# Optimization experiments

Measured on AMD Instinct MI355X. Metric: run time of the kernel, lower is better.

## Reference

```python
import jax, jax.numpy as jnp
import numpy as np

N, E, G = 50000, 500000, 2048
HID, H, ED, L = 128, 4, 12, 8
D = HID // H
EPS_BN = 1e-5


def setup_inputs() -> dict:
    key = jax.random.key(0)
    ks = jax.random.split(key, 32)
    s = 0.05
    x = jax.random.normal(ks[0], (N, 22), jnp.float32)
    src = jax.random.randint(ks[1], (E,), 0, N)
    off = jax.random.randint(ks[2], (E,), 1, N)
    dst = (src + off) % N  # guaranteed no self-loops -> move_mask is all True
    batch = jnp.sort(jax.random.randint(ks[3], (N,), 0, G))
    edge_attr = jax.random.normal(ks[4], (E, ED), jnp.float32)
    params = dict(
        Win=jax.random.normal(ks[5], (22, HID), jnp.float32) * s,
        b_in=jnp.zeros((HID,), jnp.float32),
        Wl=jax.random.normal(ks[6], (L, HID, HID), jnp.float32) * s,
        bl=jnp.zeros((L, HID), jnp.float32),
        Wr=jax.random.normal(ks[7], (L, HID, HID), jnp.float32) * s,
        br=jnp.zeros((L, HID), jnp.float32),
        We=jax.random.normal(ks[8], (L, ED, HID), jnp.float32) * s,
        att=jax.random.normal(ks[9], (L, H, D), jnp.float32) * s,
        bo=jnp.zeros((L, HID), jnp.float32),
        gamma=jnp.ones((L, HID), jnp.float32),
        beta=jnp.zeros((L, HID), jnp.float32),
        Wv1=jax.random.normal(ks[10], (HID, 64), jnp.float32) * s,
        bv1=jnp.zeros((64,), jnp.float32),
        Wv2=jax.random.normal(ks[11], (64, 3), jnp.float32) * s,
        bv2=jnp.zeros((3,), jnp.float32),
        Wp1=jax.random.normal(ks[12], (2 * HID + ED, 64), jnp.float32) * s,
        bp1=jnp.zeros((64,), jnp.float32),
        Wp2=jax.random.normal(ks[13], (64, 1), jnp.float32) * s,
        bp2=jnp.zeros((1,), jnp.float32),
    )
    return dict(x=x, src=src, dst=dst, batch=batch, edge_attr=edge_attr, **params)


def _bn(h, g, b):
    mu = h.mean(0)
    var = h.var(0)
    return (h - mu) * jax.lax.rsqrt(var + EPS_BN) * g + b


def _gatv2(h, src, dst, edge_attr, Wl, bl, Wr, br, We, att, bo):
    xl = (h @ Wl + bl).reshape(N, H, D)   # source-side (values + score)
    xr = (h @ Wr + br).reshape(N, H, D)   # target-side (score)
    e = (edge_attr @ We).reshape(E, H, D)
    sc = xl[src] + xr[dst] + e            # [E,H,D]
    sc = jnp.where(sc > 0, sc, 0.2 * sc)  # LeakyReLU(0.2)
    a = jnp.einsum('ehd,hd->eh', sc, att)  # [E,H]
    m = jax.ops.segment_max(a, dst, num_segments=N)
    ex = jnp.exp(a - m[dst])
    den = jax.ops.segment_sum(ex, dst, num_segments=N)
    alpha = ex / (den[dst] + 1e-16)        # per-destination softmax
    out = jax.ops.segment_sum(xl[src] * alpha[..., None], dst, num_segments=N)
    return out.reshape(N, HID) + bo


def reference(x, src, dst, batch, edge_attr, Win, b_in, Wl, bl, Wr, br, We, att,
              bo, gamma, beta, Wv1, bv1, Wv2, bv2, Wp1, bp1, Wp2, bp2):
    h = jax.nn.relu(x @ Win + b_in)
    for blk in range(L // 2):
        i, j = 2 * blk, 2 * blk + 1
        res = h
        h = jax.nn.relu(_bn(_gatv2(h, src, dst, edge_attr, Wl[i], bl[i], Wr[i], br[i], We[i], att[i], bo[i]), gamma[i], beta[i]))
        h = _bn(_gatv2(h, src, dst, edge_attr, Wl[j], bl[j], Wr[j], br[j], We[j], att[j], bo[j]), gamma[j], beta[j])
        h = jax.nn.relu(h + res)
    cnt = jax.ops.segment_sum(jnp.ones((N,), h.dtype), batch, num_segments=G)
    pooled = jax.ops.segment_sum(h, batch, num_segments=G) / jnp.maximum(cnt, 1.0)[:, None]
    value_logits = jax.nn.relu(pooled @ Wv1 + bv1) @ Wv2 + bv2   # [G,3]
    edge_in = jnp.concatenate([h[src], h[dst], edge_attr], axis=1)  # [E, 2*HID+ED]
    policy_logits = (jax.nn.relu(edge_in @ Wp1 + bp1) @ Wp2 + bp2)[:, 0]  # [E]
    return (value_logits, policy_logits)
```

## Files before the change

kernel.cpp:

```cpp
#include <hip/hip_runtime.h>
#include <math.h>

#define N_NODES 50000
#define N_EDGES 500000
#define N_GRAPHS 2048
#define HID 128
#define EDIM 12
#define NLAYERS 8
#define EPS_BN 1e-5f
#define LOG2E 1.44269504088896340736f

typedef __attribute__((ext_vector_type(8))) short short8;
typedef __attribute__((ext_vector_type(4))) float f32x4;
typedef __attribute__((ext_vector_type(2))) float f32x2;
typedef unsigned int uint;
typedef unsigned short ushort;

__device__ inline ushort f2bf(float x) {
  unsigned u = __float_as_uint(x);
  u = (u + 0x7FFFu + ((u >> 16) & 1u)) >> 16;
  return (ushort)u;
}
__device__ inline unsigned pk_bf16(float a, float b) {
  return (unsigned)f2bf(a) | ((unsigned)f2bf(b) << 16);
}
__device__ inline float bflo(uint q) { return __uint_as_float(q << 16); }
__device__ inline float bfhi(uint q) { return __uint_as_float(q & 0xFFFF0000u); }
__device__ inline f32x2 pfma(f32x2 a, f32x2 b, f32x2 c) {
  return __builtin_elementwise_fma(a, b, c);
}
template <int CTRL>
__device__ inline float dpp_add(float v) {
  int s = __builtin_amdgcn_update_dpp(0, __float_as_int(v), CTRL, 0xF, 0xF, true);
  return v + __int_as_float(s);
}
#define RED8(v)               \
  v = dpp_add<0xB1>(v);       \
  v = dpp_add<0x4E>(v);       \
  v = dpp_add<0x141>(v);

__global__ void zero_kernel(int* deg, int* cursor, float* stats, uint* erec) {
  int i = blockIdx.x * 256 + threadIdx.x;
  if (i < N_NODES) { deg[i] = 0; cursor[i] = 0; }
  if (i < NLAYERS * 256) stats[i] = 0.f;
  if (i < 32) erec[(size_t)N_EDGES * 8 + i] = 0u;
}

__global__ void count_kernel(const int* __restrict__ dst, int* __restrict__ deg) {
  int e = blockIdx.x * 256 + threadIdx.x;
  if (e < N_EDGES) atomicAdd(&deg[dst[e]], 1);
}

__global__ void scan1_kernel(int* __restrict__ off, int* __restrict__ bsum) {
  __shared__ int s[256];
  int t = threadIdx.x; int n = blockIdx.x * 256 + t;
  int x = (n < N_NODES) ? off[n] : 0;
  s[t] = x; __syncthreads();
  for (int o = 1; o < 256; o <<= 1) {
    int v = (t >= o) ? s[t - o] : 0;
    __syncthreads(); s[t] += v; __syncthreads();
  }
  if (n < N_NODES) off[n] = s[t] - x;
  if (t == 255) bsum[blockIdx.x] = s[255];
}

__global__ void scan2_kernel(int* __restrict__ bsum, int nb) {
  __shared__ int s[256];
  int t = threadIdx.x;
  int x = (t < nb) ? bsum[t] : 0;
  s[t] = x; __syncthreads();
  for (int o = 1; o < 256; o <<= 1) {
    int v = (t >= o) ? s[t - o] : 0;
    __syncthreads(); s[t] += v; __syncthreads();
  }
  if (t < nb) bsum[t] = s[t] - x;
}

__global__ void scan3_kernel(int* __restrict__ off, const int* __restrict__ bsum) {
  int t = threadIdx.x; int n = blockIdx.x * 256 + t;
  if (n < N_NODES) off[n] += bsum[blockIdx.x];
  if (n == 0 && blockIdx.x == 0) off[N_NODES] = N_EDGES;
}

__global__ void scatter_kernel(const int* __restrict__ src, const int* __restrict__ dst,
                               const float* __restrict__ ea,
                               const int* __restrict__ off, int* __restrict__ cursor,
                               uint* __restrict__ erec) {
  int e = blockIdx.x * 256 + threadIdx.x;
  if (e < N_EDGES) {
    int d = dst[e];
    int p = atomicAdd(&cursor[d], 1);
    int pos = off[d] + p;
    const float* eap = &ea[(size_t)e * EDIM];
    float4 e0 = *(const float4*)eap;
    float4 e1 = *(const float4*)(eap + 4);
    float4 e2 = *(const float4*)(eap + 8);
    uint4 q0, q1;
    q0.x = (uint)src[e]; q0.y = 0u;
    q0.z = pk_bf16(e0.x, e0.y); q0.w = pk_bf16(e0.z, e0.w);
    q1.x = pk_bf16(e1.x, e1.y); q1.y = pk_bf16(e1.z, e1.w);
    q1.z = pk_bf16(e2.x, e2.y); q1.w = pk_bf16(e2.z, e2.w);
    uint* o = &erec[(size_t)pos * 8];
    *(uint4*)o = q0;
    *(uint4*)(o + 4) = q1;
  }
}

__global__ void wprep_kernel(const float* __restrict__ Wl, const float* __restrict__ Wr,
                             ushort* __restrict__ wpk) {
  int idx = blockIdx.x * 256 + threadIdx.x;
  if (idx >= NLAYERS * 4 * 256 * 32) return;
  int kk = idx & 31;
  int cc = (idx >> 5) & 255;
  int kb = (idx >> 13) & 3;
  int layer = idx >> 15;
  int k = kb * 32 + kk;
  float v = (cc < 128) ? Wl[((size_t)layer * 128 + k) * 128 + cc]
                       : Wr[((size_t)layer * 128 + k) * 128 + (cc - 128)];
  wpk[idx] = f2bf(v);
}

__global__ void wprep_pol_kernel(const float* __restrict__ Wp1, ushort* __restrict__ wppk) {
  int idx = blockIdx.x * 256 + threadIdx.x;
  if (idx >= 4 * 128 * 32) return;
  int kk = idx & 31;
  int cc = (idx >> 5) & 127;
  int kb = idx >> 12;
  int k = kb * 32 + kk;
  float v = (cc < 64) ? Wp1[(size_t)k * 64 + cc] : Wp1[(size_t)(128 + k) * 64 + (cc - 64)];
  wppk[idx] = f2bf(v);
}

__global__ void inproj_kernel(const float* __restrict__ x, const float* __restrict__ Win,
                              const float* __restrict__ b_in, float* __restrict__ h,
                              ushort* __restrict__ h16) {
  __shared__ float xs[44];
  int t = threadIdx.x;
  int n0 = blockIdx.x * 2;
  if (t < 44) xs[t] = x[n0 * 22 + t];
  __syncthreads();
  int c = t & 127, half = t >> 7;
  int n = n0 + half;
  if (n < N_NODES) {
    float acc = b_in[c];
#pragma unroll
    for (int k = 0; k < 22; k++) acc = fmaf(xs[half * 22 + k], Win[k * HID + c], acc);
    float v = fmaxf(acc, 0.f);
    h[(size_t)n * HID + c] = v;
    h16[(size_t)n * HID + c] = f2bf(v);
  }
}

template <int NOUT, int SPLIT, bool BIAS, bool OUTBF16, bool BNFUSE, bool RESID, bool WRITEH>
__global__ __launch_bounds__(256) void gemm_mfma_kernel(
    const ushort* __restrict__ A16, const ushort* __restrict__ T16,
    const float* __restrict__ stats, const float* __restrict__ gamma,
    const float* __restrict__ beta, const float* __restrict__ res,
    float* __restrict__ hout,
    const ushort* __restrict__ Wpk, const float* __restrict__ b1,
    const float* __restrict__ b2, void* __restrict__ C1v, void* __restrict__ C2v,
    int nrows) {
  __shared__ ushort As[64][136];
  int t = threadIdx.x;
  int brow = blockIdx.x * 64;
  if constexpr (!BNFUSE) {
#pragma unroll
    for (int i = 0; i < 4; i++) {
      int f = t + i * 256;
      int r = f >> 4, cg = (f & 15) * 8;
      int g = brow + r;
      uint4 v = make_uint4(0, 0, 0, 0);
      if (g < nrows) v = *(const uint4*)&A16[(size_t)g * HID + cg];
      *(uint4*)&As[r][cg] = v;
    }
  } else {
    int cg = (t & 31) * 4;
    int r0 = t >> 5;
    const float invN = 1.f / (float)N_NODES;
    float4 sm = *(const float4*)&stats[cg];
    float4 sq = *(const float4*)&stats[128 + cg];
    float4 gm = *(const float4*)&gamma[cg];
    float4 bt = *(const float4*)&beta[cg];
    float s4[4] = {sm.x, sm.y, sm.z, sm.w};
    float q4[4] = {sq.x, sq.y, sq.z, sq.w};
    float g4[4] = {gm.x, gm.y, gm.z, gm.w};
    float bb4[4] = {bt.x, bt.y, bt.z, bt.w};
    float scl[4], shf[4];
#pragma unroll
    for (int k = 0; k < 4; k++) {
      float mu = s4[k] * invN;
      float var = q4[k] * invN - mu * mu;
      float rs = rsqrtf(var + EPS_BN);
      scl[k] = g4[k] * rs;
      shf[k] = bb4[k] - mu * scl[k];
    }
#pragma unroll
    for (int rr = 0; rr < 8; rr++) {
      int r = r0 + rr * 8;
      int g = brow + r;
      uint2 tvu = make_uint2(0u, 0u);
      if (g < nrows) tvu = *(const uint2*)&T16[(size_t)g * HID + cg];
      float o0 = fmaf(bflo(tvu.x), scl[0], shf[0]);
      float o1 = fmaf(bfhi(tvu.x), scl[1], shf[1]);
      float o2 = fmaf(bflo(tvu.y), scl[2], shf[2]);
      float o3 = fmaf(bfhi(tvu.y), scl[3], shf[3]);
      if constexpr (RESID) {
        if (g < nrows) {
          float4 rv = *(const float4*)&res[(size_t)g * HID + cg];
          o0 += rv.x; o1 += rv.y; o2 += rv.z; o3 += rv.w;
        }
      }
      o0 = fmaxf(o0, 0.f); o1 = fmaxf(o1, 0.f);
      o2 = fmaxf(o2, 0.f); o3 = fmaxf(o3, 0.f);
      if constexpr (WRITEH) {
        if (g < nrows) {
          float4 ov = make_float4(o0, o1, o2, o3);
          *(float4*)&hout[(size_t)g * HID + cg] = ov;
        }
      }
      *(uint2*)&As[r][cg] = make_uint2(pk_bf16(o0, o1), pk_bf16(o2, o3));
    }
  }
  __syncthreads();
  int lane = t & 63, wave = t >> 6;
  int arow = wave * 16 + (lane & 15);
  int k8 = (lane >> 4) * 8;
  constexpr int NT = NOUT / 16;
  f32x4 acc[NT];
#pragma unroll
  for (int n = 0; n < NT; n++) acc[n] = (f32x4){0.f, 0.f, 0.f, 0.f};
#pragma unroll
  for (int kb = 0; kb < 4; kb++) {
    short8 a = *(const short8*)&As[arow][kb * 32 + k8];
#pragma unroll
    for (int n = 0; n < NT; n++) {
      int col = n * 16 + (lane & 15);
      short8 b = *(const short8*)&Wpk[((size_t)(kb * NOUT + col)) * 32 + k8];
      acc[n] = __builtin_amdgcn_mfma_f32_16x16x32_bf16(a, b, acc[n], 0, 0, 0);
    }
  }
  int rbase = brow + wave * 16 + (lane >> 4) * 4;
  int ccol = lane & 15;
#pragma unroll
  for (int n = 0; n < NT; n++) {
    int col = n * 16 + ccol;
    float bias = 0.f;
    if (BIAS) bias = (col < SPLIT) ? b1[col] : b2[col - SPLIT];
    int colw = (col < SPLIT) ? col : col - SPLIT;
#pragma unroll
    for (int j = 0; j < 4; j++) {
      int row = rbase + j;
      if (row < nrows) {
        float v = acc[n][j] + bias;
        if (OUTBF16) {
          ushort* dstp = (ushort*)((col < SPLIT) ? C1v : C2v);
          dstp[(size_t)row * SPLIT + colw] = f2bf(v);
        } else {
          float* dstp = (float*)((col < SPLIT) ? C1v : C2v);
          dstp[(size_t)row * SPLIT + colw] = v;
        }
      }
    }
  }
}

#define GAT_EDGE4(ra, rb, xw, OKEXPR)                                        \
  {                                                                          \
    f32x2 xa01 = (f32x2){bflo(xw.x), bfhi(xw.x)};                            \
    f32x2 xa23 = (f32x2){bflo(xw.y), bfhi(xw.y)};                            \
    f32x2 ep01 = xa01 + xr01;                                                \
    f32x2 ep23 = xa23 + xr23;                                                \
    uint q; float lo, hi;                                                    \
    q = ra.z; lo = bflo(q); hi = bfhi(q);                                    \
    ep01 = pfma((f32x2){lo, lo}, wk01[0], ep01);                             \
    ep23 = pfma((f32x2){lo, lo}, wk23[0], ep23);                             \
    ep01 = pfma((f32x2){hi, hi}, wk01[1], ep01);                             \
    ep23 = pfma((f32x2){hi, hi}, wk23[1], ep23);                             \
    q = ra.w; lo = bflo(q); hi = bfhi(q);                                    \
    ep01 = pfma((f32x2){lo, lo}, wk01[2], ep01);                             \
    ep23 = pfma((f32x2){lo, lo}, wk23[2], ep23);                             \
    ep01 = pfma((f32x2){hi, hi}, wk01[3], ep01);                             \
    ep23 = pfma((f32x2){hi, hi}, wk23[3], ep23);                             \
    q = rb.x; lo = bflo(q); hi = bfhi(q);                                    \
    ep01 = pfma((f32x2){lo, lo}, wk01[4], ep01);                             \
    ep23 = pfma((f32x2){lo, lo}, wk23[4], ep23);                             \
    ep01 = pfma((f32x2){hi, hi}, wk01[5], ep01);                             \
    ep23 = pfma((f32x2){hi, hi}, wk23[5], ep23);                             \
    q = rb.y; lo = bflo(q); hi = bfhi(q);                                    \
    ep01 = pfma((f32x2){lo, lo}, wk01[6], ep01);                             \
    ep23 = pfma((f32x2){lo, lo}, wk23[6], ep23);                             \
    ep01 = pfma((f32x2){hi, hi}, wk01[7], ep01);                             \
    ep23 = pfma((f32x2){hi, hi}, wk23[7], ep23);                             \
    q = rb.z; lo = bflo(q); hi = bfhi(q);                                    \
    ep01 = pfma((f32x2){lo, lo}, wk01[8], ep01);                             \
    ep23 = pfma((f32x2){lo, lo}, wk23[8], ep23);                             \
    ep01 = pfma((f32x2){hi, hi}, wk01[9], ep01);                             \
    ep23 = pfma((f32x2){hi, hi}, wk23[9], ep23);                             \
    q = rb.w; lo = bflo(q); hi = bfhi(q);                                    \
    ep01 = pfma((f32x2){lo, lo}, wk01[10], ep01);                            \
    ep23 = pfma((f32x2){lo, lo}, wk23[10], ep23);                            \
    ep01 = pfma((f32x2){hi, hi}, wk01[11], ep01);                            \
    ep23 = pfma((f32x2){hi, hi}, wk23[11], ep23);                            \
    f32x2 s01 = __builtin_elementwise_max(ep01, ep01 * (f32x2){0.2f, 0.2f}); \
    f32x2 s23 = __builtin_elementwise_max(ep23, ep23 * (f32x2){0.2f, 0.2f}); \
    float v = fmaf(s01.x, at4.x,                                             \
              fmaf(s01.y, at4.y, fmaf(s23.x, at4.z, s23.y * at4.w)));        \
    RED8(v)                                                                  \
    bool ok = (OKEXPR);                                                      \
    float dm = v - m;                                                        \
    float e = __builtin_amdgcn_exp2f(-fabsf(dm));                            \
    bool big = dm > 0.f;                                                     \
    float sc = (big && ok) ? e : 1.f;                                        \
    float p = ok ? (big ? 1.f : e) : 0.f;                                    \
    m = (ok && big) ? v : m;                                                 \
    d = fmaf(d, sc, p);                                                      \
    acc01 = pfma(acc01, (f32x2){sc, sc}, (f32x2){p, p} * xa01);              \
    acc23 = pfma(acc23, (f32x2){sc, sc}, (f32x2){p, p} * xa23);              \
  }

__global__ __launch_bounds__(256, 4) void gat_kernel(
    const ushort* __restrict__ xl16, const ushort* __restrict__ xr16,
    const uint* __restrict__ erec, const int* __restrict__ off,
    const float* __restrict__ Wel, const float* __restrict__ attl,
    const float* __restrict__ bol, ushort* __restrict__ out16) {
  int lane = threadIdx.x & 63;
  int node = blockIdx.x * 4 + (threadIdx.x >> 6);
  if (node >= N_NODES) return;
  int half = lane >> 5;
  int c0 = (lane & 31) * 4;

  f32x2 wk01[12], wk23[12];
#pragma unroll
  for (int k = 0; k < 12; k++) {
    float4 w = *(const float4*)&Wel[k * HID + c0];
    wk01[k] = (f32x2){w.x, w.y};
    wk23[k] = (f32x2){w.z, w.w};
  }
  float4 at4 = *(const float4*)&attl[c0];
  at4.x *= LOG2E; at4.y *= LOG2E; at4.z *= LOG2E; at4.w *= LOG2E;
  uint2 xru = *(const uint2*)&xr16[((uint)node << 7) + c0];
  f32x2 xr01 = (f32x2){bflo(xru.x), bfhi(xru.x)};
  f32x2 xr23 = (f32x2){bflo(xru.y), bfhi(xru.y)};

  int is = off[node], deg = off[node + 1] - is;

  float m = -INFINITY, d = 0.f;
  f32x2 acc01 = (f32x2){0.f, 0.f};
  f32x2 acc23 = (f32x2){0.f, 0.f};

  if (deg > 0) {
    const uint* pe = erec + ((size_t)is + half) * 8;
    uint4 Ra = *(const uint4*)pe, Rb = *(const uint4*)(pe + 4);
    uint2 xw = *(const uint2*)&xl16[(Ra.x << 7) + c0];
    int full = deg >> 1;
    for (int i = 0; i < full; i++) {
      const uint* pn = pe + 16;
      uint4 Na = *(const uint4*)pn, Nb = *(const uint4*)(pn + 4);
      uint2 xn = *(const uint2*)&xl16[(Na.x << 7) + c0];
      GAT_EDGE4(Ra, Rb, xw, true)
      Ra = Na; Rb = Nb; xw = xn; pe = pn;
    }
    if (deg & 1) GAT_EDGE4(Ra, Rb, xw, half == 0)
  }

  float mo = __shfl_xor(m, 32);
  float dd = __shfl_xor(d, 32);
  f32x2 o01, o23;
  o01.x = __shfl_xor(acc01.x, 32); o01.y = __shfl_xor(acc01.y, 32);
  o23.x = __shfl_xor(acc23.x, 32); o23.y = __shfl_xor(acc23.y, 32);
  float mn = fmaxf(m, mo);
  float wS = (m > -INFINITY) ? __builtin_amdgcn_exp2f(m - mn) : 0.f;
  float wO = (mo > -INFINITY) ? __builtin_amdgcn_exp2f(mo - mn) : 0.f;
  float den = d * wS + dd * wO;
  f32x2 a01 = acc01 * (f32x2){wS, wS} + o01 * (f32x2){wO, wO};
  f32x2 a23 = acc23 * (f32x2){wS, wS} + o23 * (f32x2){wO, wO};
  float inv = 1.f / (den + 1e-16f);
  if (half == 0) {
    float4 bo = *(const float4*)&bol[c0];
    uint2 o;
    o.x = pk_bf16(fmaf(a01.x, inv, bo.x), fmaf(a01.y, inv, bo.y));
    o.y = pk_bf16(fmaf(a23.x, inv, bo.z), fmaf(a23.y, inv, bo.w));
    *(uint2*)&out16[((uint)node << 7) + c0] = o;
  }
}

__global__ void bnstats_kernel(const ushort* __restrict__ t16, float* __restrict__ sums) {
  int tid = threadIdx.x;
  int c2 = (tid & 63) * 2;
  int grp = tid >> 6;
  float s0 = 0.f, s1 = 0.f, q0 = 0.f, q1 = 0.f;
  for (int n = blockIdx.x * 4 + grp; n < N_NODES; n += 1024) {
    uint v = *(const uint*)&t16[((uint)n << 7) + c2];
    float a = bflo(v), b = bfhi(v);
    s0 += a; q0 = fmaf(a, a, q0);
    s1 += b; q1 = fmaf(b, b, q1);
  }
  __shared__ float ls[4][128], lq[4][128];
  *(float2*)&ls[grp][c2] = make_float2(s0, s1);
  *(float2*)&lq[grp][c2] = make_float2(q0, q1);
  __syncthreads();
  if (tid < 128) {
    float s = ls[0][tid] + ls[1][tid] + ls[2][tid] + ls[3][tid];
    atomicAdd(&sums[tid], s);
    float q = lq[0][tid] + lq[1][tid] + lq[2][tid] + lq[3][tid];
    atomicAdd(&sums[128 + tid], q);
  }
}

__global__ __launch_bounds__(256) void policy_kernel(
    const ushort* __restrict__ Ps, const ushort* __restrict__ Pd,
    const int* __restrict__ src, const int* __restrict__ dst,
    const float* __restrict__ edge_attr, const float* __restrict__ Wp1e,
    const float* __restrict__ bp1, const float* __restrict__ Wp2,
    const float* __restrict__ bp2, float* __restrict__ outp) {
  int j = threadIdx.x & 15;
  int gid = (blockIdx.x * 256 + threadIdx.x) >> 4;
  int ngroups = (gridDim.x * 256) >> 4;
  float4 we[12];
#pragma unroll
  for (int k = 0; k < 12; k++) we[k] = *(const float4*)&Wp1e[k * 64 + j * 4];
  float4 b4 = *(const float4*)&bp1[j * 4];
  float4 w2 = *(const float4*)&Wp2[j * 4];
  float bp2c = bp2[0];
  for (int e = gid; e < N_EDGES; e += ngroups) {
    int s = src[e], d = dst[e];
    const float* eap = &edge_attr[(size_t)e * EDIM];
    float4 e0 = *(const float4*)eap;
    float4 e1 = *(const float4*)(eap + 4);
    float4 e2 = *(const float4*)(eap + 8);
    uint2 psu = *(const uint2*)&Ps[(size_t)s * 64 + j * 4];
    uint2 pdu = *(const uint2*)&Pd[(size_t)d * 64 + j * 4];
    float eav[12] = {e0.x, e0.y, e0.z, e0.w, e1.x, e1.y, e1.z, e1.w, e2.x, e2.y, e2.z, e2.w};
    float hx = bflo(psu.x) + bflo(pdu.x) + b4.x;
    float hy = bfhi(psu.x) + bfhi(pdu.x) + b4.y;
    float hz = bflo(psu.y) + bflo(pdu.y) + b4.z;
    float hw = bfhi(psu.y) + bfhi(pdu.y) + b4.w;
#pragma unroll
    for (int k = 0; k < 12; k++) {
      hx = fmaf(eav[k], we[k].x, hx);
      hy = fmaf(eav[k], we[k].y, hy);
      hz = fmaf(eav[k], we[k].z, hz);
      hw = fmaf(eav[k], we[k].w, hw);
    }
    hx = fmaxf(hx, 0.f); hy = fmaxf(hy, 0.f); hz = fmaxf(hz, 0.f); hw = fmaxf(hw, 0.f);
    float v = fmaf(hx, w2.x, fmaf(hy, w2.y, fmaf(hz, w2.z, hw * w2.w)));
    v += __shfl_xor(v, 1);
    v += __shfl_xor(v, 2);
    v += __shfl_xor(v, 4);
    v += __shfl_xor(v, 8);
    if (j == 0) outp[e] = v + bp2c;
  }
}

__device__ int lower_bound_dev(const int* a, int n, int key) {
  int lo = 0, hi = n;
  while (lo < hi) {
    int mid = (lo + hi) >> 1;
    if (a[mid] < key) lo = mid + 1; else hi = mid;
  }
  return lo;
}

__global__ void poolvalue_kernel(const float* __restrict__ h, const int* __restrict__ batch,
                                 const float* __restrict__ Wv1, const float* __restrict__ bv1,
                                 const float* __restrict__ Wv2, const float* __restrict__ bv2,
                                 float* __restrict__ outv) {
  __shared__ float pl[128];
  __shared__ float hd[64];
  __shared__ int range[2];
  int g = blockIdx.x, t = threadIdx.x;
  if (t == 0) {
    range[0] = lower_bound_dev(batch, N_NODES, g);
    range[1] = lower_bound_dev(batch, N_NODES, g + 1);
  }
  __syncthreads();
  int lo = range[0], hi = range[1];
  float s = 0.f;
  for (int n = lo; n < hi; n++) s += h[(size_t)n * HID + t];
  float cnt = (float)(hi - lo);
  pl[t] = s / fmaxf(cnt, 1.f);
  __syncthreads();
  if (t < 64) {
    float a = bv1[t];
    for (int c = 0; c < 128; c++) a = fmaf(pl[c], Wv1[c * 64 + t], a);
    hd[t] = fmaxf(a, 0.f);
  }
  __syncthreads();
  if (t < 3) {
    float a = bv2[t];
    for (int j = 0; j < 64; j++) a = fmaf(hd[j], Wv2[j * 3 + t], a);
    outv[g * 3 + t] = a;
  }
}

extern "C" void kernel_launch(void* const* d_in, const int* in_sizes, int n_in,
                              void* d_out, int out_size, void* d_ws, size_t ws_size,
                              hipStream_t stream) {
  (void)in_sizes; (void)n_in; (void)out_size; (void)ws_size;
  const float* x    = (const float*)d_in[0];
  const int*   src  = (const int*)d_in[1];
  const int*   dst  = (const int*)d_in[2];
  const int*   batch= (const int*)d_in[3];
  const float* ea   = (const float*)d_in[4];
  const float* Win  = (const float*)d_in[5];
  const float* b_in = (const float*)d_in[6];
  const float* Wl   = (const float*)d_in[7];
  const float* bl   = (const float*)d_in[8];
  const float* Wr   = (const float*)d_in[9];
  const float* br   = (const float*)d_in[10];
  const float* We   = (const float*)d_in[11];
  const float* att  = (const float*)d_in[12];
  const float* bo   = (const float*)d_in[13];
  const float* gamma= (const float*)d_in[14];
  const float* beta = (const float*)d_in[15];
  const float* Wv1  = (const float*)d_in[16];
  const float* bv1  = (const float*)d_in[17];
  const float* Wv2  = (const float*)d_in[18];
  const float* bv2  = (const float*)d_in[19];
  const float* Wp1  = (const float*)d_in[20];
  const float* bp1  = (const float*)d_in[21];
  const float* Wp2  = (const float*)d_in[22];
  const float* bp2  = (const float*)d_in[23];

  float* outv = (float*)d_out;
  float* outp = outv + (size_t)N_GRAPHS * 3;

  float* hres   = (float*)d_ws;
  ushort* tmp16 = (ushort*)(hres + (size_t)N_NODES * HID);
  ushort* h16   = tmp16 + (size_t)N_NODES * HID;
  ushort* xl16  = h16 + (size_t)N_NODES * HID;
  ushort* xr16  = xl16 + (size_t)N_NODES * HID;
  float* stats  = (float*)(xr16 + (size_t)N_NODES * HID);
  ushort* wpk   = (ushort*)(stats + NLAYERS * 256);
  ushort* wppk  = wpk + (size_t)NLAYERS * 4 * 256 * 32;
  int* off    = (int*)(wppk + 4 * 128 * 32);
  int* cursor = off + (N_NODES + 1);
  int* bsum   = cursor + N_NODES;
  uint* erec  = (uint*)(((uintptr_t)(bsum + 256) + 15) & ~(uintptr_t)15);

  const int NB = (N_NODES + 255) / 256;
  const int EB = (N_EDGES + 255) / 256;

  zero_kernel<<<NB, 256, 0, stream>>>(off, cursor, stats, erec);
  count_kernel<<<EB, 256, 0, stream>>>(dst, off);
  scan1_kernel<<<NB, 256, 0, stream>>>(off, bsum);
  scan2_kernel<<<1, 256, 0, stream>>>(bsum, NB);
  scan3_kernel<<<NB, 256, 0, stream>>>(off, bsum);
  scatter_kernel<<<EB, 256, 0, stream>>>(src, dst, ea, off, cursor, erec);
  wprep_kernel<<<(NLAYERS * 4 * 256 * 32 + 255) / 256, 256, 0, stream>>>(Wl, Wr, wpk);
  wprep_pol_kernel<<<(4 * 128 * 32 + 255) / 256, 256, 0, stream>>>(Wp1, wppk);
  inproj_kernel<<<N_NODES / 2, 256, 0, stream>>>(x, Win, b_in, hres, h16);

  const int MB = (N_NODES + 63) / 64;
  const int GATB = (N_NODES + 3) / 4;

  for (int l = 0; l < NLAYERS; l++) {
    if (l == 0) {
      gemm_mfma_kernel<256, 128, true, true, false, false, false><<<MB, 256, 0, stream>>>(
          h16, nullptr, nullptr, nullptr, nullptr, nullptr, nullptr,
          wpk, bl, br, xl16, xr16, N_NODES);
    } else if (l & 1) {
      int p = l - 1;
      gemm_mfma_kernel<256, 128, true, true, true, false, false><<<MB, 256, 0, stream>>>(
          nullptr, tmp16, stats + p * 256, gamma + p * HID, beta + p * HID, nullptr, nullptr,
          wpk + (size_t)l * 32768, bl + l * HID, br + l * HID, xl16, xr16, N_NODES);
    } else {
      int p = l - 1;
      gemm_mfma_kernel<256, 128, true, true, true, true, true><<<MB, 256, 0, stream>>>(
          nullptr, tmp16, stats + p * 256, gamma + p * HID, beta + p * HID, hres, hres,
          wpk + (size_t)l * 32768, bl + l * HID, br + l * HID, xl16, xr16, N_NODES);
    }
    gat_kernel<<<GATB, 256, 0, stream>>>(xl16, xr16, erec, off,
                                         We + (size_t)l * EDIM * HID, att + (size_t)l * HID,
                                         bo + (size_t)l * HID, tmp16);
    bnstats_kernel<<<256, 256, 0, stream>>>(tmp16, stats + l * 256);
  }

  ushort* Ps = xl16;
  ushort* Pd = xr16;
  gemm_mfma_kernel<128, 64, false, true, true, true, true><<<MB, 256, 0, stream>>>(
      nullptr, tmp16, stats + 7 * 256, gamma + 7 * HID, beta + 7 * HID, hres, hres,
      wppk, nullptr, nullptr, Ps, Pd, N_NODES);
  policy_kernel<<<2048, 256, 0, stream>>>(Ps, Pd, src, dst, ea,
                                          Wp1 + 256 * 64, bp1, Wp2, bp2, outp);
  poolvalue_kernel<<<N_GRAPHS, 128, 0, stream>>>(hres, batch, Wv1, bv1, Wv2, bv2, outv);
}
```

Measured before the change: 1.240 ms.

## Process four edges per wavefront in GAT kernel with 8 channels per lane

```diff
diff --git a/kernel.cpp b/kernel.cpp
--- a/kernel.cpp
+++ b/kernel.cpp
@@ -34,10 +34,9 @@
   int s = __builtin_amdgcn_update_dpp(0, __float_as_int(v), CTRL, 0xF, 0xF, true);
   return v + __int_as_float(s);
 }
-#define RED8(v)               \
+#define RED4(v)               \
   v = dpp_add<0xB1>(v);       \
-  v = dpp_add<0x4E>(v);       \
-  v = dpp_add<0x141>(v);
+  v = dpp_add<0x4E>(v);
 
 __global__ void zero_kernel(int* deg, int* cursor, float* stats, uint* erec) {
   int i = blockIdx.x * 256 + threadIdx.x;
@@ -264,48 +263,57 @@
   }
 }
 
-#define GAT_EDGE4(ra, rb, xw, OKEXPR)                                        \
+#define GAT_EDGE8(ra, rb, xw, OKEXPR)                                        \
   {                                                                          \
     f32x2 xa01 = (f32x2){bflo(xw.x), bfhi(xw.x)};                            \
     f32x2 xa23 = (f32x2){bflo(xw.y), bfhi(xw.y)};                            \
+    f32x2 xa45 = (f32x2){bflo(xw.z), bfhi(xw.z)};                            \
+    f32x2 xa67 = (f32x2){bflo(xw.w), bfhi(xw.w)};                            \
     f32x2 ep01 = xa01 + xr01;                                                \
     f32x2 ep23 = xa23 + xr23;                                                \
-    uint q; float lo, hi;                                                    \
-    q = ra.z; lo = bflo(q); hi = bfhi(q);                                    \
-    ep01 = pfma((f32x2){lo, lo}, wk01[0], ep01);                             \
-    ep23 = pfma((f32x2){lo, lo}, wk23[0], ep23);                             \
-    ep01 = pfma((f32x2){hi, hi}, wk01[1], ep01);                             \
-    ep23 = pfma((f32x2){hi, hi}, wk23[1], ep23);                             \
-    q = ra.w; lo = bflo(q); hi = bfhi(q);                                    \
-    ep01 = pfma((f32x2){lo, lo}, wk01[2], ep01);                             \
-    ep23 = pfma((f32x2){lo, lo}, wk23[2], ep23);                             \
-    ep01 = pfma((f32x2){hi, hi}, wk01[3], ep01);                             \
-    ep23 = pfma((f32x2){hi, hi}, wk23[3], ep23);                             \
-    q = rb.x; lo = bflo(q); hi = bfhi(q);                                    \
-    ep01 = pfma((f32x2){lo, lo}, wk01[4], ep01);                             \
-    ep23 = pfma((f32x2){lo, lo}, wk23[4], ep23);                             \
-    ep01 = pfma((f32x2){hi, hi}, wk01[5], ep01);                             \
-    ep23 = pfma((f32x2){hi, hi}, wk23[5], ep23);                             \
-    q = rb.y; lo = bflo(q); hi = bfhi(q);                                    \
-    ep01 = pfma((f32x2){lo, lo}, wk01[6], ep01);                             \
-    ep23 = pfma((f32x2){lo, lo}, wk23[6], ep23);                             \
-    ep01 = pfma((f32x2){hi, hi}, wk01[7], ep01);                             \
-    ep23 = pfma((f32x2){hi, hi}, wk23[7], ep23);                             \
-    q = rb.z; lo = bflo(q); hi = bfhi(q);                                    \
-    ep01 = pfma((f32x2){lo, lo}, wk01[8], ep01);                             \
-    ep23 = pfma((f32x2){lo, lo}, wk23[8], ep23);                             \
-    ep01 = pfma((f32x2){hi, hi}, wk01[9], ep01);                             \
-    ep23 = pfma((f32x2){hi, hi}, wk23[9], ep23);                             \
-    q = rb.w; lo = bflo(q); hi = bfhi(q);                                    \
-    ep01 = pfma((f32x2){lo, lo}, wk01[10], ep01);                            \
-    ep23 = pfma((f32x2){lo, lo}, wk23[10], ep23);                            \
-    ep01 = pfma((f32x2){hi, hi}, wk01[11], ep01);                            \
-    ep23 = pfma((f32x2){hi, hi}, wk23[11], ep23);                            \
+    f32x2 ep45 = xa45 + xr45;                                                \
+    f32x2 ep67 = xa67 + xr67;                                                \
+    uint q; f32x2 bl, bh;                                                    \
+    q = ra.z; bl = (f32x2){bflo(q), bflo(q)}; bh = (f32x2){bfhi(q), bfhi(q)};\
+    ep01 = pfma(bl, wkg0[0], ep01); ep23 = pfma(bl, wkg1[0], ep23);          \
+    ep45 = pfma(bl, wkg2[0], ep45); ep67 = pfma(bl, wkg3[0], ep67);          \
+    ep01 = pfma(bh, wkg0[1], ep01); ep23 = pfma(bh, wkg1[1], ep23);          \
+    ep45 = pfma(bh, wkg2[1], ep45); ep67 = pfma(bh, wkg3[1], ep67);          \
+    q = ra.w; bl = (f32x2){bflo(q), bflo(q)}; bh = (f32x2){bfhi(q), bfhi(q)};\
+    ep01 = pfma(bl, wkg0[2], ep01); ep23 = pfma(bl, wkg1[2], ep23);          \
+    ep45 = pfma(bl, wkg2[2], ep45); ep67 = pfma(bl, wkg3[2], ep67);          \
+    ep01 = pfma(bh, wkg0[3], ep01); ep23 = pfma(bh, wkg1[3], ep23);          \
+    ep45 = pfma(bh, wkg2[3], ep45); ep67 = pfma(bh, wkg3[3], ep67);          \
+    q = rb.x; bl = (f32x2){bflo(q), bflo(q)}; bh = (f32x2){bfhi(q), bfhi(q)};\
+    ep01 = pfma(bl, wkg0[4], ep01); ep23 = pfma(bl, wkg1[4], ep23);          \
+    ep45 = pfma(bl, wkg2[4], ep45); ep67 = pfma(bl, wkg3[4], ep67);          \
+    ep01 = pfma(bh, wkg0[5], ep01); ep23 = pfma(bh, wkg1[5], ep23);          \
+    ep45 = pfma(bh, wkg2[5], ep45); ep67 = pfma(bh, wkg3[5], ep67);          \
+    q = rb.y; bl = (f32x2){bflo(q), bflo(q)}; bh = (f32x2){bfhi(q), bfhi(q)};\
+    ep01 = pfma(bl, wkg0[6], ep01); ep23 = pfma(bl, wkg1[6], ep23);          \
+    ep45 = pfma(bl, wkg2[6], ep45); ep67 = pfma(bl, wkg3[6], ep67);          \
+    ep01 = pfma(bh, wkg0[7], ep01); ep23 = pfma(bh, wkg1[7], ep23);          \
+    ep45 = pfma(bh, wkg2[7], ep45); ep67 = pfma(bh, wkg3[7], ep67);          \
+    q = rb.z; bl = (f32x2){bflo(q), bflo(q)}; bh = (f32x2){bfhi(q), bfhi(q)};\
+    ep01 = pfma(bl, wkg0[8], ep01); ep23 = pfma(bl, wkg1[8], ep23);          \
+    ep45 = pfma(bl, wkg2[8], ep45); ep67 = pfma(bl, wkg3[8], ep67);          \
+    ep01 = pfma(bh, wkg0[9], ep01); ep23 = pfma(bh, wkg1[9], ep23);          \
+    ep45 = pfma(bh, wkg2[9], ep45); ep67 = pfma(bh, wkg3[9], ep67);          \
+    q = rb.w; bl = (f32x2){bflo(q), bflo(q)}; bh = (f32x2){bfhi(q), bfhi(q)};\
+    ep01 = pfma(bl, wkg0[10], ep01); ep23 = pfma(bl, wkg1[10], ep23);        \
+    ep45 = pfma(bl, wkg2[10], ep45); ep67 = pfma(bl, wkg3[10], ep67);        \
+    ep01 = pfma(bh, wkg0[11], ep01); ep23 = pfma(bh, wkg1[11], ep23);        \
+    ep45 = pfma(bh, wkg2[11], ep45); ep67 = pfma(bh, wkg3[11], ep67);        \
     f32x2 s01 = __builtin_elementwise_max(ep01, ep01 * (f32x2){0.2f, 0.2f}); \
     f32x2 s23 = __builtin_elementwise_max(ep23, ep23 * (f32x2){0.2f, 0.2f}); \
-    float v = fmaf(s01.x, at4.x,                                             \
-              fmaf(s01.y, at4.y, fmaf(s23.x, at4.z, s23.y * at4.w)));        \
-    RED8(v)                                                                  \
+    f32x2 s45 = __builtin_elementwise_max(ep45, ep45 * (f32x2){0.2f, 0.2f}); \
+    f32x2 s67 = __builtin_elementwise_max(ep67, ep67 * (f32x2){0.2f, 0.2f}); \
+    f32x2 pv = s01 * at01;                                                   \
+    pv = pfma(s23, at23, pv);                                                \
+    pv = pfma(s45, at45, pv);                                                \
+    pv = pfma(s67, at67, pv);                                                \
+    float v = pv.x + pv.y;                                                   \
+    RED4(v)                                                                  \
     bool ok = (OKEXPR);                                                      \
     float dm = v - m;                                                        \
     float e = __builtin_amdgcn_exp2f(-fabsf(dm));                            \
@@ -314,73 +322,98 @@
     float p = ok ? (big ? 1.f : e) : 0.f;                                    \
     m = (ok && big) ? v : m;                                                 \
     d = fmaf(d, sc, p);                                                      \
-    acc01 = pfma(acc01, (f32x2){sc, sc}, (f32x2){p, p} * xa01);              \
-    acc23 = pfma(acc23, (f32x2){sc, sc}, (f32x2){p, p} * xa23);              \
-  }
-
-__global__ __launch_bounds__(256, 4) void gat_kernel(
+    f32x2 scv = (f32x2){sc, sc}, pvv = (f32x2){p, p};                        \
+    acc01 = pfma(acc01, scv, pvv * xa01);                                    \
+    acc23 = pfma(acc23, scv, pvv * xa23);                                    \
+    acc45 = pfma(acc45, scv, pvv * xa45);                                    \
+    acc67 = pfma(acc67, scv, pvv * xa67);                                    \
+  }
+
+__global__ __launch_bounds__(64) void gat_kernel(
     const ushort* __restrict__ xl16, const ushort* __restrict__ xr16,
     const uint* __restrict__ erec, const int* __restrict__ off,
     const float* __restrict__ Wel, const float* __restrict__ attl,
     const float* __restrict__ bol, ushort* __restrict__ out16) {
-  int lane = threadIdx.x & 63;
-  int node = blockIdx.x * 4 + (threadIdx.x >> 6);
-  if (node >= N_NODES) return;
-  int half = lane >> 5;
-  int c0 = (lane & 31) * 4;
-
-  f32x2 wk01[12], wk23[12];
+  int lane = threadIdx.x;
+  int node = blockIdx.x;
+  int quad = lane >> 4;
+  int c0 = (lane & 15) * 8;
+
+  f32x2 wkg0[12], wkg1[12], wkg2[12], wkg3[12];
 #pragma unroll
   for (int k = 0; k < 12; k++) {
-    float4 w = *(const float4*)&Wel[k * HID + c0];
-    wk01[k] = (f32x2){w.x, w.y};
-    wk23[k] = (f32x2){w.z, w.w};
-  }
-  float4 at4 = *(const float4*)&attl[c0];
-  at4.x *= LOG2E; at4.y *= LOG2E; at4.z *= LOG2E; at4.w *= LOG2E;
-  uint2 xru = *(const uint2*)&xr16[((uint)node << 7) + c0];
+    float4 a = *(const float4*)&Wel[k * HID + c0];
+    float4 b = *(const float4*)&Wel[k * HID + c0 + 4];
+    wkg0[k] = (f32x2){a.x, a.y};
+    wkg1[k] = (f32x2){a.z, a.w};
+    wkg2[k] = (f32x2){b.x, b.y};
+    wkg3[k] = (f32x2){b.z, b.w};
+  }
+  float4 ata = *(const float4*)&attl[c0];
+  float4 atb = *(const float4*)&attl[c0 + 4];
+  f32x2 at01 = (f32x2){ata.x * LOG2E, ata.y * LOG2E};
+  f32x2 at23 = (f32x2){ata.z * LOG2E, ata.w * LOG2E};
+  f32x2 at45 = (f32x2){atb.x * LOG2E, atb.y * LOG2E};
+  f32x2 at67 = (f32x2){atb.z * LOG2E, atb.w * LOG2E};
+  uint4 xru = *(const uint4*)&xr16[((uint)node << 7) + c0];
   f32x2 xr01 = (f32x2){bflo(xru.x), bfhi(xru.x)};
   f32x2 xr23 = (f32x2){bflo(xru.y), bfhi(xru.y)};
+  f32x2 xr45 = (f32x2){bflo(xru.z), bfhi(xru.z)};
+  f32x2 xr67 = (f32x2){bflo(xru.w), bfhi(xru.w)};
 
   int is = off[node], deg = off[node + 1] - is;
 
   float m = -INFINITY, d = 0.f;
   f32x2 acc01 = (f32x2){0.f, 0.f};
   f32x2 acc23 = (f32x2){0.f, 0.f};
+  f32x2 acc45 = (f32x2){0.f, 0.f};
+  f32x2 acc67 = (f32x2){0.f, 0.f};
 
   if (deg > 0) {
-    const uint* pe = erec + ((size_t)is + half) * 8;
+    const uint* pe = erec + ((size_t)(is + quad)) * 8;
     uint4 Ra = *(const uint4*)pe, Rb = *(const uint4*)(pe + 4);
-    uint2 xw = *(const uint2*)&xl16[(Ra.x << 7) + c0];
-    int full = deg >> 1;
+    uint4 xw = *(const uint4*)&xl16[(Ra.x << 7) + c0];
+    int full = deg >> 2;
     for (int i = 0; i < full; i++) {
-      const uint* pn = pe + 16;
+      const uint* pn = pe + 32;
       uint4 Na = *(const uint4*)pn, Nb = *(const uint4*)(pn + 4);
-      uint2 xn = *(const uint2*)&xl16[(Na.x << 7) + c0];
-      GAT_EDGE4(Ra, Rb, xw, true)
+      uint4 xn = *(const uint4*)&xl16[(Na.x << 7) + c0];
+      GAT_EDGE8(Ra, Rb, xw, true)
       Ra = Na; Rb = Nb; xw = xn; pe = pn;
     }
-    if (deg & 1) GAT_EDGE4(Ra, Rb, xw, half == 0)
-  }
-
-  float mo = __shfl_xor(m, 32);
-  float dd = __shfl_xor(d, 32);
-  f32x2 o01, o23;
-  o01.x = __shfl_xor(acc01.x, 32); o01.y = __shfl_xor(acc01.y, 32);
-  o23.x = __shfl_xor(acc23.x, 32); o23.y = __shfl_xor(acc23.y, 32);
-  float mn = fmaxf(m, mo);
-  float wS = (m > -INFINITY) ? __builtin_amdgcn_exp2f(m - mn) : 0.f;
-  float wO = (mo > -INFINITY) ? __builtin_amdgcn_exp2f(mo - mn) : 0.f;
-  float den = d * wS + dd * wO;
-  f32x2 a01 = acc01 * (f32x2){wS, wS} + o01 * (f32x2){wO, wO};
-  f32x2 a23 = acc23 * (f32x2){wS, wS} + o23 * (f32x2){wO, wO};
-  float inv = 1.f / (den + 1e-16f);
-  if (half == 0) {
-    float4 bo = *(const float4*)&bol[c0];
-    uint2 o;
-    o.x = pk_bf16(fmaf(a01.x, inv, bo.x), fmaf(a01.y, inv, bo.y));
-    o.y = pk_bf16(fmaf(a23.x, inv, bo.z), fmaf(a23.y, inv, bo.w));
-    *(uint2*)&out16[((uint)node << 7) + c0] = o;
+    if (deg & 3) GAT_EDGE8(Ra, Rb, xw, quad < (deg & 3))
+  }
+
+#pragma unroll
+  for (int ofs = 16; ofs <= 32; ofs <<= 1) {
+    float mo = __shfl_xor(m, ofs);
+    float dd = __shfl_xor(d, ofs);
+    f32x2 o01, o23, o45, o67;
+    o01.x = __shfl_xor(acc01.x, ofs); o01.y = __shfl_xor(acc01.y, ofs);
+    o23.x = __shfl_xor(acc23.x, ofs); o23.y = __shfl_xor(acc23.y, ofs);
+    o45.x = __shfl_xor(acc45.x, ofs); o45.y = __shfl_xor(acc45.y, ofs);
+    o67.x = __shfl_xor(acc67.x, ofs); o67.y = __shfl_xor(acc67.y, ofs);
+    float mn = fmaxf(m, mo);
+    float wS = (m > -INFINITY) ? __builtin_amdgcn_exp2f(m - mn) : 0.f;
+    float wO = (mo > -INFINITY) ? __builtin_amdgcn_exp2f(mo - mn) : 0.f;
+    d = d * wS + dd * wO;
+    f32x2 wSv = (f32x2){wS, wS}, wOv = (f32x2){wO, wO};
+    acc01 = acc01 * wSv + o01 * wOv;
+    acc23 = acc23 * wSv + o23 * wOv;
+    acc45 = acc45 * wSv + o45 * wOv;
+    acc67 = acc67 * wSv + o67 * wOv;
+    m = mn;
+  }
+  float inv = 1.f / (d + 1e-16f);
+  if (lane < 16) {
+    float4 boa = *(const float4*)&bol[c0];
+    float4 bob = *(const float4*)&bol[c0 + 4];
+    uint4 o;
+    o.x = pk_bf16(fmaf(acc01.x, inv, boa.x), fmaf(acc01.y, inv, boa.y));
+    o.y = pk_bf16(fmaf(acc23.x, inv, boa.z), fmaf(acc23.y, inv, boa.w));
+    o.z = pk_bf16(fmaf(acc45.x, inv, bob.x), fmaf(acc45.y, inv, bob.y));
+    o.w = pk_bf16(fmaf(acc67.x, inv, bob.z), fmaf(acc67.y, inv, bob.w));
+    *(uint4*)&out16[((uint)node << 7) + c0] = o;
   }
 }
 
@@ -552,7 +585,6 @@
   inproj_kernel<<<N_NODES / 2, 256, 0, stream>>>(x, Win, b_in, hres, h16);
 
   const int MB = (N_NODES + 63) / 64;
-  const int GATB = (N_NODES + 3) / 4;
 
   for (int l = 0; l < NLAYERS; l++) {
     if (l == 0) {
@@ -570,9 +602,9 @@
           nullptr, tmp16, stats + p * 256, gamma + p * HID, beta + p * HID, hres, hres,
           wpk + (size_t)l * 32768, bl + l * HID, br + l * HID, xl16, xr16, N_NODES);
     }
-    gat_kernel<<<GATB, 256, 0, stream>>>(xl16, xr16, erec, off,
-                                         We + (size_t)l * EDIM * HID, att + (size_t)l * HID,
-                                         bo + (size_t)l * HID, tmp16);
+    gat_kernel<<<N_NODES, 64, 0, stream>>>(xl16, xr16, erec, off,
+                                           We + (size_t)l * EDIM * HID, att + (size_t)l * HID,
+                                           bo + (size_t)l * HID, tmp16);
     bnstats_kernel<<<256, 256, 0, stream>>>(tmp16, stats + l * 256);
   }
 
```

New measurement: 1.354 ms. 1.09x slower.
